# Kernel tuning notes

Hardware: AMD Instinct MI355X
Metric: run time of the kernel (lower is better)

The kernel has to match this reference:

```python
import jax, jax.numpy as jnp
import numpy as np

CHUNK_SIZE = 2048
EPS = 1e-12  # torch F.normalize clamps the norm at 1e-12


def _l2_normalize(x, axis):
    n = jnp.sqrt(jnp.sum(x * x, axis=axis, keepdims=True))
    return x / jnp.maximum(n, EPS)


def _nnfm_loss(F_r, F_s, chunk_size=CHUNK_SIZE):
    B, C, H_r, W_r = F_r.shape
    _, _, H_s, W_s = F_s.shape
    N_r = H_r * W_r
    N_s = H_s * W_s
    assert N_r % chunk_size == 0, "N_r must be divisible by chunk_size for this reference"
    n_chunks = N_r // chunk_size

    F_s_norm = _l2_normalize(F_s.reshape(B, C, N_s), axis=1)  # (B, C, N_s)
    F_r_flat = F_r.reshape(B, C, N_r)
    # (n_chunks, B, C, chunk) -- contiguous chunks along N_r, matching the torch loop
    chunks = F_r_flat.reshape(B, C, n_chunks, chunk_size).transpose(2, 0, 1, 3)

    def body(chunk):  # chunk: (B, C, chunk_size)
        cn = _l2_normalize(chunk, axis=1)
        sim = jnp.einsum('bcn,bcm->bnm', cn, F_s_norm)  # (B, chunk, N_s)
        # min(1 - sim) over N_s == 1 - max(sim)
        return 1.0 - jnp.max(sim, axis=2)  # (B, chunk)

    min_dists = jax.lax.map(body, chunks)  # (n_chunks, B, chunk) -- bounded memory
    return jnp.mean(min_dists)


def setup_inputs() -> dict:
    key = jax.random.key(0)
    k1, k2 = jax.random.split(key)
    F_r = jax.random.normal(k1, (1, 768, 128, 128), dtype=jnp.float32)
    F_s = jax.random.normal(k2, (1, 768, 128, 128), dtype=jnp.float32)
    return {"F_r": F_r, "F_s": F_s}


def reference(F_r, F_s):
    return _nnfm_loss(F_r, F_s)
```

## Files before the change

kernel.cpp:

```cpp
#include <hip/hip_runtime.h>
#include <cstdint>
#include <cstddef>

#define C_DIM 768
#define N_DIM 16384

typedef __attribute__((ext_vector_type(8))) short short8;
typedef __attribute__((ext_vector_type(4))) float f32x4;

__device__ __forceinline__ ushort f2bf(float f) {
    uint32_t u = __float_as_uint(f);
    uint32_t r = 0x7fffu + ((u >> 16) & 1u);
    return (ushort)((u + r) >> 16);
}

__device__ __forceinline__ void async_ld16(const void* g, void* l) {
    __builtin_amdgcn_global_load_lds(
        (__attribute__((address_space(1))) void*)g,
        (__attribute__((address_space(3))) void*)l,
        16, 0, 0);
}

template<int N> __device__ __forceinline__ void wait_vmcnt() {
    if constexpr (N == 4)      asm volatile("s_waitcnt vmcnt(4)" ::: "memory");
    else if constexpr (N == 2) asm volatile("s_waitcnt vmcnt(2)" ::: "memory");
    else if constexpr (N == 0) asm volatile("s_waitcnt vmcnt(0)" ::: "memory");
}

__global__ __launch_bounds__(256) void norm_tr(const float* __restrict__ F0,
                                               ushort* __restrict__ T0,
                                               const float* __restrict__ F1,
                                               ushort* __restrict__ T1) {
    const float*  F = blockIdx.y ? F1 : F0;
    ushort*       T = blockIdx.y ? T1 : T0;
    const int i0 = blockIdx.x * 64;
    const int t  = threadIdx.x;
    const int tx = t & 63;
    const int ty = t >> 6;

    float ss = 0.f;
    for (int c = ty; c < C_DIM; c += 4) {
        float v = F[(size_t)c * N_DIM + i0 + tx];
        ss += v * v;
    }
    __shared__ float red[4][64];
    __shared__ float scale[64];
    red[ty][tx] = ss;
    __syncthreads();
    if (t < 64) {
        float s = red[0][t] + red[1][t] + red[2][t] + red[3][t];
        float n = sqrtf(s);
        scale[t] = 1.0f / fmaxf(n, 1e-12f);
    }
    __syncthreads();

    __shared__ float tile[64][65];
    const int i_l   = t >> 3;
    const int c_off = (t & 7) * 8;
    for (int c0 = 0; c0 < C_DIM; c0 += 64) {
        #pragma unroll
        for (int rr = 0; rr < 16; ++rr) {
            int c_l = rr * 4 + ty;
            tile[c_l][tx] = F[(size_t)(c0 + c_l) * N_DIM + i0 + tx] * scale[tx];
        }
        __syncthreads();
        #pragma unroll
        for (int half = 0; half < 2; ++half) {
            int il = i_l + half * 32;
            __align__(16) ushort pack[8];
            #pragma unroll
            for (int j = 0; j < 8; ++j)
                pack[j] = f2bf(tile[c_off + j][il]);
            *(uint4*)&T[(size_t)(i0 + il) * C_DIM + c0 + c_off] = *(const uint4*)pack;
        }
        __syncthreads();
    }
}

__device__ __forceinline__ f32x4 mfma16(short8 a, short8 b, f32x4 c) {
    return __builtin_amdgcn_mfma_f32_16x16x32_bf16(a, b, c, 0, 0, 0);
}

template<bool STAGE, int W0, int W1, int W3>
__device__ __forceinline__ void half_iter(
    ushort* As, ushort* Bs,
    const ushort* agA, const ushort* bgB,
    int ktn,
    int ldst, int abase, int bbase, int aq0, int aq1,
    f32x4 (&acc)[8][4])
{
    const int ko = ktn * 64;
    short8 a03[4][2], a47[4][2], b01[2][2], b23[2][2];

    #pragma unroll
    for (int mt = 0; mt < 4; ++mt) {
        a03[mt][0] = *(const short8*)(As + abase + mt * 1024 + aq0);
        a03[mt][1] = *(const short8*)(As + abase + mt * 1024 + aq1);
    }
    #pragma unroll
    for (int nt = 0; nt < 2; ++nt) {
        b01[nt][0] = *(const short8*)(Bs + bbase + nt * 1024 + aq0);
        b01[nt][1] = *(const short8*)(Bs + bbase + nt * 1024 + aq1);
    }
    __builtin_amdgcn_s_barrier();
    asm volatile("s_waitcnt lgkmcnt(0)" ::: "memory");
    __builtin_amdgcn_sched_barrier(0);
    __builtin_amdgcn_s_setprio(1);
    #pragma unroll
    for (int mt = 0; mt < 4; ++mt)
        #pragma unroll
        for (int nt = 0; nt < 2; ++nt) {
            acc[mt][nt] = mfma16(a03[mt][0], b01[nt][0], acc[mt][nt]);
            acc[mt][nt] = mfma16(a03[mt][1], b01[nt][1], acc[mt][nt]);
        }
    __builtin_amdgcn_s_setprio(0);
    wait_vmcnt<W0>();
    __builtin_amdgcn_s_barrier();

    #pragma unroll
    for (int nt = 0; nt < 2; ++nt) {
        b23[nt][0] = *(const short8*)(Bs + 8192 + bbase + nt * 1024 + aq0);
        b23[nt][1] = *(const short8*)(Bs + 8192 + bbase + nt * 1024 + aq1);
    }
    if constexpr (STAGE) {
        async_ld16(agA + ko,                 As + ldst);
        async_ld16(agA + ko + 128 * C_DIM,   As + 8192 + ldst);
        async_ld16(bgB + ko,                 Bs + ldst);
        async_ld16(bgB + ko + 128 * C_DIM,   Bs + 4096 + ldst);
    }
    __builtin_amdgcn_s_barrier();
    asm volatile("s_waitcnt lgkmcnt(0)" ::: "memory");
    __builtin_amdgcn_sched_barrier(0);
    __builtin_amdgcn_s_setprio(1);
    #pragma unroll
    for (int mt = 0; mt < 4; ++mt)
        #pragma unroll
        for (int nt = 0; nt < 2; ++nt) {
            acc[mt][2 + nt] = mfma16(a03[mt][0], b23[nt][0], acc[mt][2 + nt]);
            acc[mt][2 + nt] = mfma16(a03[mt][1], b23[nt][1], acc[mt][2 + nt]);
        }
    __builtin_amdgcn_s_setprio(0);
    wait_vmcnt<W1>();
    __builtin_amdgcn_s_barrier();

    #pragma unroll
    for (int mt = 0; mt < 4; ++mt) {
        a47[mt][0] = *(const short8*)(As + 4096 + abase + mt * 1024 + aq0);
        a47[mt][1] = *(const short8*)(As + 4096 + abase + mt * 1024 + aq1);
    }
    if constexpr (STAGE) {
        async_ld16(bgB + ko + 32 * C_DIM,    Bs + 8192 + ldst);
        async_ld16(bgB + ko + 160 * C_DIM,   Bs + 12288 + ldst);
    }
    __builtin_amdgcn_s_barrier();
    asm volatile("s_waitcnt lgkmcnt(0)" ::: "memory");
    __builtin_amdgcn_sched_barrier(0);
    __builtin_amdgcn_s_setprio(1);
    #pragma unroll
    for (int mt = 0; mt < 4; ++mt)
        #pragma unroll
        for (int nt = 0; nt < 2; ++nt) {
            acc[4 + mt][nt] = mfma16(a47[mt][0], b01[nt][0], acc[4 + mt][nt]);
            acc[4 + mt][nt] = mfma16(a47[mt][1], b01[nt][1], acc[4 + mt][nt]);
        }
    __builtin_amdgcn_s_setprio(0);
    __builtin_amdgcn_s_barrier();

    if constexpr (STAGE) {
        async_ld16(agA + ko + 64 * C_DIM,    As + 4096 + ldst);
        async_ld16(agA + ko + 192 * C_DIM,   As + 12288 + ldst);
    }
    __builtin_amdgcn_s_barrier();
    __builtin_amdgcn_s_setprio(1);
    #pragma unroll
    for (int mt = 0; mt < 4; ++mt)
        #pragma unroll
        for (int nt = 0; nt < 2; ++nt) {
            acc[4 + mt][2 + nt] = mfma16(a47[mt][0], b23[nt][0], acc[4 + mt][2 + nt]);
            acc[4 + mt][2 + nt] = mfma16(a47[mt][1], b23[nt][1], acc[4 + mt][2 + nt]);
        }
    __builtin_amdgcn_s_setprio(0);
    wait_vmcnt<W3>();
    __builtin_amdgcn_s_barrier();
}

__global__ __launch_bounds__(512, 2) void gemm_rowmax(const ushort* __restrict__ A,
                                                      const ushort* __restrict__ B,
                                                      unsigned* __restrict__ rowkey) {
    __shared__ __align__(16) ushort As[16384];
    __shared__ __align__(16) ushort Bs[16384];

    const int t    = threadIdx.x;
    const int lane = t & 63;
    const int w    = t >> 6;
    const int wm   = w >> 2;
    const int wn   = w & 3;

    const int bid   = blockIdx.x;
    const int xcd   = bid & 7;
    const int local = bid >> 3;
    const int m0    = (local >> 3) * 256;
    const int n0    = (xcd * 8 + (local & 7)) * 256;

    f32x4 acc[8][4];
    #pragma unroll
    for (int i = 0; i < 8; ++i)
        #pragma unroll
        for (int j = 0; j < 4; ++j)
            acc[i][j] = (f32x4){0.f, 0.f, 0.f, 0.f};

    const int srow = t >> 3;
    const int schk = ((t & 7) ^ (srow & 7)) * 8;
    const ushort* agA = A + (size_t)(m0 + srow) * C_DIM + schk;
    const int brow = ((t >> 8) & 1) * 64 + (srow & 31);
    const ushort* bgB = B + (size_t)(n0 + brow) * C_DIM + schk;
    const int ldst = t * 8;

    const int aq0   = ((lane >> 4) ^ (lane & 7)) * 8;
    const int aq1   = (((lane >> 4) + 4) ^ (lane & 7)) * 8;
    const int abase = wm * 8192 + (lane & 15) * 64;
    const int bbase = wn * 2048 + (lane & 15) * 64;

    async_ld16(agA,                 As + ldst);
    async_ld16(agA + 128 * C_DIM,   As + 8192 + ldst);
    async_ld16(bgB,                 Bs + ldst);
    async_ld16(bgB + 128 * C_DIM,   Bs + 4096 + ldst);
    async_ld16(bgB + 32 * C_DIM,    Bs + 8192 + ldst);
    async_ld16(bgB + 160 * C_DIM,   Bs + 12288 + ldst);
    async_ld16(agA + 64 * C_DIM,    As + 4096 + ldst);
    async_ld16(agA + 192 * C_DIM,   As + 12288 + ldst);
    wait_vmcnt<4>();
    __builtin_amdgcn_s_barrier();

    #pragma unroll 1
    for (int j = 0; j < 11; ++j)
        half_iter<true, 2, 4, 4>(As, Bs, agA, bgB, j + 1,
                                 ldst, abase, bbase, aq0, aq1, acc);
    half_iter<false, 2, 0, -1>(As, Bs, agA, bgB, 0,
                               ldst, abase, bbase, aq0, aq1, acc);

    #pragma unroll
    for (int mt = 0; mt < 8; ++mt) {
        #pragma unroll
        for (int reg = 0; reg < 4; ++reg) {
            float v = fmaxf(fmaxf(acc[mt][0][reg], acc[mt][1][reg]),
                            fmaxf(acc[mt][2][reg], acc[mt][3][reg]));
            #pragma unroll
            for (int off = 1; off < 16; off <<= 1)
                v = fmaxf(v, __shfl_xor(v, off, 64));
            if ((lane & 15) == 0) {
                int m = m0 + wm * 128 + mt * 16 + (lane >> 4) * 4 + reg;
                unsigned u = __float_as_uint(v);
                u = (u & 0x80000000u) ? ~u : (u | 0x80000000u);
                atomicMax(&rowkey[m], u);
            }
        }
    }
}

__global__ __launch_bounds__(1024) void finalize(const unsigned* __restrict__ rowkey,
                                                 float* __restrict__ out) {
    const int t = threadIdx.x;
    float s = 0.f;
    for (int i = t; i < N_DIM; i += 1024) {
        unsigned u = rowkey[i];
        float f = (u & 0x80000000u) ? __uint_as_float(u ^ 0x80000000u)
                                    : __uint_as_float(~u);
        s += f;
    }
    #pragma unroll
    for (int off = 32; off >= 1; off >>= 1)
        s += __shfl_down(s, off, 64);
    __shared__ float part[16];
    if ((t & 63) == 0) part[t >> 6] = s;
    __syncthreads();
    if (t == 0) {
        float tot = 0.f;
        #pragma unroll
        for (int i = 0; i < 16; ++i) tot += part[i];
        out[0] = 1.0f - tot * (1.0f / (float)N_DIM);
    }
}

extern "C" void kernel_launch(void* const* d_in, const int* in_sizes, int n_in,
                              void* d_out, int out_size, void* d_ws, size_t ws_size,
                              hipStream_t stream) {
    const float* F_r = (const float*)d_in[0];
    const float* F_s = (const float*)d_in[1];

    ushort*   Rt     = (ushort*)d_ws;
    ushort*   St     = Rt + (size_t)N_DIM * C_DIM;
    unsigned* rowkey = (unsigned*)(St + (size_t)N_DIM * C_DIM);
    float*    out    = (float*)d_out;

    hipLaunchKernelGGL(norm_tr, dim3(N_DIM / 64, 2), dim3(256), 0, stream,
                       F_r, Rt, F_s, St);
    hipMemsetAsync(rowkey, 0, N_DIM * sizeof(unsigned), stream);
    hipLaunchKernelGGL(gemm_rowmax, dim3((N_DIM / 256) * (N_DIM / 256)), dim3(512),
                       0, stream, Rt, St, rowkey);
    hipLaunchKernelGGL(finalize, dim3(1), dim3(1024), 0, stream, rowkey, out);
}
```

Baseline: 820.8 us.

## Software-pipeline LDS fragment reads across phases in bf16 GEMM rowmax

Restructures the GEMM main loop so LDS fragment reads for the next phase are issued before the current MFMA block. The A03/B01 fragments for the next k-step are prefetched at the end of the previous iteration and kept in registers across calls, and several barriers and lgkmcnt waits are removed. The aim is to hide LDS latency behind MFMA work and cut barrier stalls. In exchange, register pressure rises under the 512x2 launch bounds, and the reworked vmcnt/barrier ordering risks races on the shared buffers.

Result: faster. 735.1 us (-10.4%).

```diff
diff --git a/kernel.cpp b/kernel.cpp
--- a/kernel.cpp
+++ b/kernel.cpp
@@ -19,12 +19,6 @@
         (__attribute__((address_space(1))) void*)g,
         (__attribute__((address_space(3))) void*)l,
         16, 0, 0);
-}
-
-template<int N> __device__ __forceinline__ void wait_vmcnt() {
-    if constexpr (N == 4)      asm volatile("s_waitcnt vmcnt(4)" ::: "memory");
-    else if constexpr (N == 2) asm volatile("s_waitcnt vmcnt(2)" ::: "memory");
-    else if constexpr (N == 0) asm volatile("s_waitcnt vmcnt(0)" ::: "memory");
 }
 
 __global__ __launch_bounds__(256) void norm_tr(const float* __restrict__ F0,
@@ -81,46 +75,41 @@
     return __builtin_amdgcn_mfma_f32_16x16x32_bf16(a, b, c, 0, 0, 0);
 }
 
-template<bool STAGE, int W0, int W1, int W3>
+template<bool STAGE, bool READNEXT>
 __device__ __forceinline__ void half_iter(
     ushort* As, ushort* Bs,
     const ushort* agA, const ushort* bgB,
     int ktn,
     int ldst, int abase, int bbase, int aq0, int aq1,
+    short8 (&a03)[4][2], short8 (&a47)[4][2],
+    short8 (&b01)[2][2], short8 (&b23)[2][2],
     f32x4 (&acc)[8][4])
 {
     const int ko = ktn * 64;
-    short8 a03[4][2], a47[4][2], b01[2][2], b23[2][2];
-
-    #pragma unroll
-    for (int mt = 0; mt < 4; ++mt) {
-        a03[mt][0] = *(const short8*)(As + abase + mt * 1024 + aq0);
-        a03[mt][1] = *(const short8*)(As + abase + mt * 1024 + aq1);
-    }
-    #pragma unroll
-    for (int nt = 0; nt < 2; ++nt) {
-        b01[nt][0] = *(const short8*)(Bs + bbase + nt * 1024 + aq0);
-        b01[nt][1] = *(const short8*)(Bs + bbase + nt * 1024 + aq1);
-    }
-    __builtin_amdgcn_s_barrier();
-    asm volatile("s_waitcnt lgkmcnt(0)" ::: "memory");
-    __builtin_amdgcn_sched_barrier(0);
-    __builtin_amdgcn_s_setprio(1);
-    #pragma unroll
-    for (int mt = 0; mt < 4; ++mt)
-        #pragma unroll
-        for (int nt = 0; nt < 2; ++nt) {
-            acc[mt][nt] = mfma16(a03[mt][0], b01[nt][0], acc[mt][nt]);
-            acc[mt][nt] = mfma16(a03[mt][1], b01[nt][1], acc[mt][nt]);
-        }
-    __builtin_amdgcn_s_setprio(0);
-    wait_vmcnt<W0>();
-    __builtin_amdgcn_s_barrier();
 
     #pragma unroll
     for (int nt = 0; nt < 2; ++nt) {
         b23[nt][0] = *(const short8*)(Bs + 8192 + bbase + nt * 1024 + aq0);
         b23[nt][1] = *(const short8*)(Bs + 8192 + bbase + nt * 1024 + aq1);
+    }
+    __builtin_amdgcn_sched_barrier(0);
+    __builtin_amdgcn_s_setprio(1);
+    #pragma unroll
+    for (int mt = 0; mt < 4; ++mt)
+        #pragma unroll
+        for (int nt = 0; nt < 2; ++nt) {
+            acc[mt][nt] = mfma16(a03[mt][0], b01[nt][0], acc[mt][nt]);
+            acc[mt][nt] = mfma16(a03[mt][1], b01[nt][1], acc[mt][nt]);
+        }
+    __builtin_amdgcn_s_setprio(0);
+    asm volatile("s_waitcnt vmcnt(0)" ::: "memory");
+    __builtin_amdgcn_s_barrier();
+    __builtin_amdgcn_sched_barrier(0);
+
+    #pragma unroll
+    for (int mt = 0; mt < 4; ++mt) {
+        a47[mt][0] = *(const short8*)(As + 4096 + abase + mt * 1024 + aq0);
+        a47[mt][1] = *(const short8*)(As + 4096 + abase + mt * 1024 + aq1);
     }
     if constexpr (STAGE) {
         async_ld16(agA + ko,                 As + ldst);
@@ -128,8 +117,6 @@
         async_ld16(bgB + ko,                 Bs + ldst);
         async_ld16(bgB + ko + 128 * C_DIM,   Bs + 4096 + ldst);
     }
-    __builtin_amdgcn_s_barrier();
-    asm volatile("s_waitcnt lgkmcnt(0)" ::: "memory");
     __builtin_amdgcn_sched_barrier(0);
     __builtin_amdgcn_s_setprio(1);
     #pragma unroll
@@ -140,20 +127,13 @@
             acc[mt][2 + nt] = mfma16(a03[mt][1], b23[nt][1], acc[mt][2 + nt]);
         }
     __builtin_amdgcn_s_setprio(0);
-    wait_vmcnt<W1>();
-    __builtin_amdgcn_s_barrier();
-
-    #pragma unroll
-    for (int mt = 0; mt < 4; ++mt) {
-        a47[mt][0] = *(const short8*)(As + 4096 + abase + mt * 1024 + aq0);
-        a47[mt][1] = *(const short8*)(As + 4096 + abase + mt * 1024 + aq1);
-    }
+    __builtin_amdgcn_s_barrier();
+    __builtin_amdgcn_sched_barrier(0);
+
     if constexpr (STAGE) {
         async_ld16(bgB + ko + 32 * C_DIM,    Bs + 8192 + ldst);
         async_ld16(bgB + ko + 160 * C_DIM,   Bs + 12288 + ldst);
     }
-    __builtin_amdgcn_s_barrier();
-    asm volatile("s_waitcnt lgkmcnt(0)" ::: "memory");
     __builtin_amdgcn_sched_barrier(0);
     __builtin_amdgcn_s_setprio(1);
     #pragma unroll
@@ -164,13 +144,28 @@
             acc[4 + mt][nt] = mfma16(a47[mt][1], b01[nt][1], acc[4 + mt][nt]);
         }
     __builtin_amdgcn_s_setprio(0);
-    __builtin_amdgcn_s_barrier();
-
+    if constexpr (STAGE)
+        asm volatile("s_waitcnt vmcnt(2)" ::: "memory");
+    __builtin_amdgcn_s_barrier();
+    __builtin_amdgcn_sched_barrier(0);
+
+    if constexpr (READNEXT) {
+        #pragma unroll
+        for (int mt = 0; mt < 4; ++mt) {
+            a03[mt][0] = *(const short8*)(As + abase + mt * 1024 + aq0);
+            a03[mt][1] = *(const short8*)(As + abase + mt * 1024 + aq1);
+        }
+        #pragma unroll
+        for (int nt = 0; nt < 2; ++nt) {
+            b01[nt][0] = *(const short8*)(Bs + bbase + nt * 1024 + aq0);
+            b01[nt][1] = *(const short8*)(Bs + bbase + nt * 1024 + aq1);
+        }
+    }
     if constexpr (STAGE) {
         async_ld16(agA + ko + 64 * C_DIM,    As + 4096 + ldst);
         async_ld16(agA + ko + 192 * C_DIM,   As + 12288 + ldst);
     }
-    __builtin_amdgcn_s_barrier();
+    __builtin_amdgcn_sched_barrier(0);
     __builtin_amdgcn_s_setprio(1);
     #pragma unroll
     for (int mt = 0; mt < 4; ++mt)
@@ -180,8 +175,10 @@
             acc[4 + mt][2 + nt] = mfma16(a47[mt][1], b23[nt][1], acc[4 + mt][2 + nt]);
         }
     __builtin_amdgcn_s_setprio(0);
-    wait_vmcnt<W3>();
-    __builtin_amdgcn_s_barrier();
+    if constexpr (STAGE)
+        asm volatile("s_waitcnt vmcnt(2)" ::: "memory");
+    __builtin_amdgcn_s_barrier();
+    __builtin_amdgcn_sched_barrier(0);
 }
 
 __global__ __launch_bounds__(512, 2) void gemm_rowmax(const ushort* __restrict__ A,
@@ -220,6 +217,8 @@
     const int aq1   = (((lane >> 4) + 4) ^ (lane & 7)) * 8;
     const int abase = wm * 8192 + (lane & 15) * 64;
     const int bbase = wn * 2048 + (lane & 15) * 64;
+
+    short8 a03[4][2], a47[4][2], b01[2][2], b23[2][2];
 
     async_ld16(agA,                 As + ldst);
     async_ld16(agA + 128 * C_DIM,   As + 8192 + ldst);
@@ -229,15 +228,32 @@
     async_ld16(bgB + 160 * C_DIM,   Bs + 12288 + ldst);
     async_ld16(agA + 64 * C_DIM,    As + 4096 + ldst);
     async_ld16(agA + 192 * C_DIM,   As + 12288 + ldst);
-    wait_vmcnt<4>();
-    __builtin_amdgcn_s_barrier();
+    asm volatile("s_waitcnt vmcnt(4)" ::: "memory");
+    __builtin_amdgcn_s_barrier();
+    __builtin_amdgcn_sched_barrier(0);
+
+    #pragma unroll
+    for (int mt = 0; mt < 4; ++mt) {
+        a03[mt][0] = *(const short8*)(As + abase + mt * 1024 + aq0);
+        a03[mt][1] = *(const short8*)(As + abase + mt * 1024 + aq1);
+    }
+    #pragma unroll
+    for (int nt = 0; nt < 2; ++nt) {
+        b01[nt][0] = *(const short8*)(Bs + bbase + nt * 1024 + aq0);
+        b01[nt][1] = *(const short8*)(Bs + bbase + nt * 1024 + aq1);
+    }
+    asm volatile("s_waitcnt vmcnt(2)" ::: "memory");
+    __builtin_amdgcn_s_barrier();
+    __builtin_amdgcn_sched_barrier(0);
 
     #pragma unroll 1
     for (int j = 0; j < 11; ++j)
-        half_iter<true, 2, 4, 4>(As, Bs, agA, bgB, j + 1,
-                                 ldst, abase, bbase, aq0, aq1, acc);
-    half_iter<false, 2, 0, -1>(As, Bs, agA, bgB, 0,
-                               ldst, abase, bbase, aq0, aq1, acc);
+        half_iter<true, true>(As, Bs, agA, bgB, j + 1,
+                              ldst, abase, bbase, aq0, aq1,
+                              a03, a47, b01, b23, acc);
+    half_iter<false, false>(As, Bs, agA, bgB, 0,
+                            ldst, abase, bbase, aq0, aq1,
+                            a03, a47, b01, b23, acc);
 
     #pragma unroll
     for (int mt = 0; mt < 8; ++mt) {
```
